# Kernel optimization log

Hardware: AMD Instinct MI355X
Metric: run time of the kernel (lower is better)

The kernel has to match this reference:

```python
import jax, jax.numpy as jnp
import numpy as np

N_SITES, N_BONDS, N_GRAPHS, D = 100000, 800000, 1000, 64
H1, H2 = 64, 32  # megnet_h1, megnet_h2


def _lin(x, w, b):
    return x @ w + b


def _relu_lin(x, w, b):
    return jax.nn.relu(_lin(x, w, b))


def _segment_mean(x, seg, num_segments):
    s = jax.ops.segment_sum(x, seg, num_segments=num_segments)
    cnt = jax.ops.segment_sum(jnp.ones((x.shape[0],), x.dtype), seg, num_segments=num_segments)
    return s / jnp.maximum(cnt, 1.0)[:, None]


def setup_inputs() -> dict:
    key = jax.random.key(0)
    ks = list(jax.random.split(key, 80))
    ki = iter(ks)

    def lp(din, dout):
        w = jax.random.normal(next(ki), (din, dout), jnp.float32) / np.sqrt(din)
        b = jax.random.normal(next(ki), (dout,), jnp.float32) * 0.01
        return w, b

    inp = {}
    inp['sites'] = jax.random.normal(next(ki), (N_SITES, D), jnp.float32)
    inp['bonds'] = jax.random.normal(next(ki), (N_BONDS, D), jnp.float32)
    inp['states'] = jax.random.normal(next(ki), (N_GRAPHS, D), jnp.float32)

    # pre-MEGNet dense layers (D -> H1(=64) -> premegnet_h2(=64))
    for name, din, dout in [('sites_fc1', D, 64), ('sites_fc2', 64, D),
                            ('bonds_fc1', D, 64), ('bonds_fc2', 64, D),
                            ('states_fc1', D, 64), ('states_fc2', 64, D)]:
        w, b = lp(din, dout)
        inp['w_' + name], inp['b_' + name] = w, b
    # bond update MLP: (2D + D + D) -> H1 -> H2 -> D
    for name, din, dout in [('bu_fc1', 4 * D, H1), ('bu_fc2', H1, H2), ('bu_fc3', H2, D)]:
        w, b = lp(din, dout)
        inp['w_' + name], inp['b_' + name] = w, b
    # site update MLP: 3D -> H1 -> H2 -> D
    for name, din, dout in [('su_fc1', 3 * D, H1), ('su_fc2', H1, H2), ('su_fc3', H2, D)]:
        w, b = lp(din, dout)
        inp['w_' + name], inp['b_' + name] = w, b
    # state update MLP: 3D -> H1 -> H2 -> D
    for name, din, dout in [('stu_fc1', 3 * D, H1), ('stu_fc2', H1, H2), ('stu_fc3', H2, D)]:
        w, b = lp(din, dout)
        inp['w_' + name], inp['b_' + name] = w, b

    inp['indices1'] = jax.random.randint(next(ki), (N_BONDS,), 0, N_SITES, jnp.int32)
    inp['indices2'] = jax.random.randint(next(ki), (N_BONDS,), 0, N_SITES, jnp.int32)
    inp['graph_to_sites'] = jnp.sort(jax.random.randint(next(ki), (N_SITES,), 0, N_GRAPHS, jnp.int32))
    inp['graph_to_bonds'] = jnp.sort(jax.random.randint(next(ki), (N_BONDS,), 0, N_GRAPHS, jnp.int32))
    return inp


def _megnet_block(sites, bonds, states,
                  w_sites_fc1, b_sites_fc1, w_sites_fc2, b_sites_fc2,
                  w_bonds_fc1, b_bonds_fc1, w_bonds_fc2, b_bonds_fc2,
                  w_states_fc1, b_states_fc1, w_states_fc2, b_states_fc2,
                  w_bu_fc1, b_bu_fc1, w_bu_fc2, b_bu_fc2, w_bu_fc3, b_bu_fc3,
                  w_su_fc1, b_su_fc1, w_su_fc2, b_su_fc2, w_su_fc3, b_su_fc3,
                  w_stu_fc1, b_stu_fc1, w_stu_fc2, b_stu_fc2, w_stu_fc3, b_stu_fc3,
                  indices1, indices2, graph_to_sites, graph_to_bonds):
    # pre-MEGNet fc layers
    sites = _relu_lin(_relu_lin(sites, w_sites_fc1, b_sites_fc1), w_sites_fc2, b_sites_fc2)
    bonds = _relu_lin(_relu_lin(bonds, w_bonds_fc1, b_bonds_fc1), w_bonds_fc2, b_bonds_fc2)
    states = _relu_lin(_relu_lin(states, w_states_fc1, b_states_fc1), w_states_fc2, b_states_fc2)
    # first_block=True: residual is taken AFTER the fc layers
    init_sites, init_bonds, init_states = sites, bonds, states

    # bond update: gather endpoints + graph state, concat, 3-layer MLP
    v = jnp.concatenate([sites[indices1], sites[indices2], bonds, states[graph_to_bonds]], axis=1)
    v = _relu_lin(v, w_bu_fc1, b_bu_fc1)
    v = _relu_lin(v, w_bu_fc2, b_bu_fc2)
    bonds_new = _relu_lin(v, w_bu_fc3, b_bu_fc3)

    # site update: mean-pool bonds onto their first endpoint
    bonds_pool = _segment_mean(bonds_new, indices1, N_SITES)
    v = jnp.concatenate([bonds_pool, sites, states[graph_to_sites]], axis=1)
    v = _relu_lin(v, w_su_fc1, b_su_fc1)
    v = _relu_lin(v, w_su_fc2, b_su_fc2)
    sites_new = _relu_lin(v, w_su_fc3, b_su_fc3)

    # state update: mean-pool bonds and sites per graph
    bonds_g = _segment_mean(bonds_new, graph_to_bonds, N_GRAPHS)
    sites_g = _segment_mean(sites_new, graph_to_sites, N_GRAPHS)
    v = jnp.concatenate([bonds_g, sites_g, states], axis=1)
    v = _relu_lin(v, w_stu_fc1, b_stu_fc1)
    v = _relu_lin(v, w_stu_fc2, b_stu_fc2)
    states_new = _relu_lin(v, w_stu_fc3, b_stu_fc3)

    return (sites_new + init_sites, bonds_new + init_bonds, states_new + init_states)


def reference(sites, bonds, states,
              w_sites_fc1, b_sites_fc1, w_sites_fc2, b_sites_fc2,
              w_bonds_fc1, b_bonds_fc1, w_bonds_fc2, b_bonds_fc2,
              w_states_fc1, b_states_fc1, w_states_fc2, b_states_fc2,
              w_bu_fc1, b_bu_fc1, w_bu_fc2, b_bu_fc2, w_bu_fc3, b_bu_fc3,
              w_su_fc1, b_su_fc1, w_su_fc2, b_su_fc2, w_su_fc3, b_su_fc3,
              w_stu_fc1, b_stu_fc1, w_stu_fc2, b_stu_fc2, w_stu_fc3, b_stu_fc3,
              indices1, indices2, graph_to_sites, graph_to_bonds):
    return _megnet_block(sites, bonds, states,
                         w_sites_fc1, b_sites_fc1, w_sites_fc2, b_sites_fc2,
                         w_bonds_fc1, b_bonds_fc1, w_bonds_fc2, b_bonds_fc2,
                         w_states_fc1, b_states_fc1, w_states_fc2, b_states_fc2,
                         w_bu_fc1, b_bu_fc1, w_bu_fc2, b_bu_fc2, w_bu_fc3, b_bu_fc3,
                         w_su_fc1, b_su_fc1, w_su_fc2, b_su_fc2, w_su_fc3, b_su_fc3,
                         w_stu_fc1, b_stu_fc1, w_stu_fc2, b_stu_fc2, w_stu_fc3, b_stu_fc3,
                         indices1, indices2, graph_to_sites, graph_to_bonds)
```

## Files before the change

kernel.cpp:

```cpp
#include <hip/hip_runtime.h>

#define N_SITES  100000
#define N_BONDS  800000
#define N_GRAPHS 1000

typedef short bfx8 __attribute__((ext_vector_type(8)));
typedef float fx4  __attribute__((ext_vector_type(4)));

__device__ __forceinline__ bfx8 ldfrag128(const short* buf, int row, int k){
  int off = (row*128 + k*2) ^ ((row&7)<<4);
  return *(const bfx8*)((const char*)buf + off);
}
__device__ __forceinline__ bfx8 ldfrag64(const short* buf, int row, int k){
  int off = (row*64 + k*2) ^ ((row&7)<<4);
  return *(const bfx8*)((const char*)buf + off);
}
__device__ __forceinline__ void stb16_128(short* buf, int row, int col, float v){
  int off = (row*128 + col*2) ^ ((row&7)<<4);
  *(__bf16*)((char*)buf + off) = (__bf16)v;
}
__device__ __forceinline__ float ldb16_128(const short* buf, int row, int col){
  int off = (row*128 + col*2) ^ ((row&7)<<4);
  return (float)*(const __bf16*)((const char*)buf + off);
}
__device__ __forceinline__ void stb16_64(short* buf, int row, int col, float v){
  int off = (row*64 + col*2) ^ ((row&7)<<4);
  *(__bf16*)((char*)buf + off) = (__bf16)v;
}

__device__ __forceinline__ void gemm64(const short* Ab, const short* Bw,
                                       fx4 (&acc)[4][4], int q, int c){
  #pragma unroll
  for (int kt = 0; kt < 2; ++kt){
    int k = kt*32 + q*8;
    bfx8 a0 = ldfrag128(Ab,  0+c, k);
    bfx8 a1 = ldfrag128(Ab, 16+c, k);
    bfx8 a2 = ldfrag128(Ab, 32+c, k);
    bfx8 a3 = ldfrag128(Ab, 48+c, k);
    #pragma unroll
    for (int nt = 0; nt < 4; ++nt){
      bfx8 b = ldfrag128(Bw, nt*16+c, k);
      acc[0][nt] = __builtin_amdgcn_mfma_f32_16x16x32_bf16(a0, b, acc[0][nt], 0,0,0);
      acc[1][nt] = __builtin_amdgcn_mfma_f32_16x16x32_bf16(a1, b, acc[1][nt], 0,0,0);
      acc[2][nt] = __builtin_amdgcn_mfma_f32_16x16x32_bf16(a2, b, acc[2][nt], 0,0,0);
      acc[3][nt] = __builtin_amdgcn_mfma_f32_16x16x32_bf16(a3, b, acc[3][nt], 0,0,0);
    }
  }
}
__device__ __forceinline__ void initbias(fx4 (&acc)[4][4], const float* B, int c){
  #pragma unroll
  for (int nt = 0; nt < 4; ++nt){
    float bv = B[nt*16+c];
    fx4 v = {bv, bv, bv, bv};
    #pragma unroll
    for (int mt = 0; mt < 4; ++mt) acc[mt][nt] = v;
  }
}
__device__ __forceinline__ void wbC128(short* dst, fx4 (&acc)[4][4], int q, int c){
  #pragma unroll
  for (int mt = 0; mt < 4; ++mt)
    #pragma unroll
    for (int nt = 0; nt < 4; ++nt)
      #pragma unroll
      for (int i = 0; i < 4; ++i)
        stb16_128(dst, mt*16+q*4+i, nt*16+c, fmaxf(acc[mt][nt][i], 0.f));
}

template<int CNT>
__device__ __forceinline__ void stage_w(float* dst, const float* __restrict__ src, int tid, int nth){
  for (int i = tid; i < CNT; i += nth) dst[i] = src[i];
}
__device__ __forceinline__ void stage_b(float* dst, const float* __restrict__ src, int n, int tid){
  if (tid < n) dst[tid] = src[tid];
}

template<int K, int N, int R, int XS>
__device__ __forceinline__ void layerR(const float* __restrict__ W,
                                       const float* __restrict__ x,
                                       float* __restrict__ acc, int j)
{
  #pragma unroll
  for (int k = 0; k < K; k += 4){
    float w0 = W[(k+0)*N + j];
    float w1 = W[(k+1)*N + j];
    float w2 = W[(k+2)*N + j];
    float w3 = W[(k+3)*N + j];
    #pragma unroll
    for (int r = 0; r < R; ++r){
      float4 xv = *(const float4*)(x + r*XS + k);
      acc[r] = fmaf(xv.x, w0, acc[r]);
      acc[r] = fmaf(xv.y, w1, acc[r]);
      acc[r] = fmaf(xv.z, w2, acc[r]);
      acc[r] = fmaf(xv.w, w3, acc[r]);
    }
  }
}

__device__ __forceinline__ int lbound(const int* __restrict__ a, int n, int v){
  int lo = 0, hi = n;
  while (lo < hi){ int m = (lo+hi) >> 1; if (a[m] < v) lo = m+1; else hi = m; }
  return lo;
}

__global__ __launch_bounds__(256) void prep_small_kernel(
    const float* __restrict__ states,
    const float* __restrict__ w1, const float* __restrict__ b1,
    const float* __restrict__ w2, const float* __restrict__ b2,
    const float* __restrict__ w_bu1, const float* __restrict__ b_bu1,
    const float* __restrict__ w_su1, const float* __restrict__ b_su1,
    const float* __restrict__ w_stu1, const float* __restrict__ b_stu1,
    float* __restrict__ states2, float* __restrict__ statec_bu,
    float* __restrict__ statec_su, float* __restrict__ statec_stu)
{
  __shared__ float W1[4096], W2[4096], WD[4096], WsuC[4096], WstuC[4096];
  __shared__ float B1[64], B2[64], Bbu[64], Bsu[64], Bstu[64];
  __shared__ alignas(16) float xs[4][64];
  __shared__ alignas(16) float hs[4][64];
  int tid = threadIdx.x;
  stage_w<4096>(W1,    w1,              tid, 256);
  stage_w<4096>(W2,    w2,              tid, 256);
  stage_w<4096>(WD,    w_bu1 + 192*64,  tid, 256);
  stage_w<4096>(WsuC,  w_su1 + 128*64,  tid, 256);
  stage_w<4096>(WstuC, w_stu1 + 128*64, tid, 256);
  stage_b(B1, b1, 64, tid);  stage_b(B2, b2, 64, tid);
  stage_b(Bbu, b_bu1, 64, tid); stage_b(Bsu, b_su1, 64, tid); stage_b(Bstu, b_stu1, 64, tid);
  __syncthreads();
  int w = tid >> 6, lane = tid & 63;
  int g = blockIdx.x*4 + w;
  xs[w][lane] = states[(size_t)g*64 + lane];
  float a = B1[lane];
  layerR<64,64,1,64>(W1, xs[w], &a, lane);
  hs[w][lane] = fmaxf(a, 0.f);
  a = B2[lane];
  layerR<64,64,1,64>(W2, hs[w], &a, lane);
  float s2 = fmaxf(a, 0.f);
  xs[w][lane] = s2;
  size_t o = (size_t)g*64 + lane;
  float abu = Bbu[lane], asu = Bsu[lane], astu = Bstu[lane];
  layerR<64,64,1,64>(WD,    xs[w], &abu,  lane);
  layerR<64,64,1,64>(WsuC,  xs[w], &asu,  lane);
  layerR<64,64,1,64>(WstuC, xs[w], &astu, lane);
  states2[o]    = s2;
  statec_bu[o]  = abu;
  statec_su[o]  = asu;
  statec_stu[o] = astu;
}

__global__ __launch_bounds__(256) void sites_pre_kernel(
    const float* __restrict__ sites,
    const float* __restrict__ w1, const float* __restrict__ b1,
    const float* __restrict__ w2, const float* __restrict__ b2,
    float* __restrict__ sites2)
{
  __shared__ float W1[4096], W2[4096];
  __shared__ float B1[64], B2[64];
  __shared__ alignas(16) float xs[4][4][64];
  __shared__ alignas(16) float hs[4][4][64];
  int tid = threadIdx.x;
  stage_w<4096>(W1, w1, tid, 256);
  stage_w<4096>(W2, w2, tid, 256);
  stage_b(B1, b1, 64, tid); stage_b(B2, b2, 64, tid);
  __syncthreads();
  int w = tid >> 6, lane = tid & 63;
  int wgid = blockIdx.x*4 + w;
  for (int n = 0; n < 7; ++n){
    int G = n*4096 + wgid;
    if (G >= 25000) break;
    #pragma unroll
    for (int r = 0; r < 4; ++r)
      xs[w][r][lane] = sites[((size_t)(4*G + r))*64 + lane];
    {
      float a[4] = {B1[lane], B1[lane], B1[lane], B1[lane]};
      layerR<64,64,4,64>(W1, &xs[w][0][0], a, lane);
      #pragma unroll
      for (int r = 0; r < 4; ++r) hs[w][r][lane] = fmaxf(a[r], 0.f);
    }
    {
      float a[4] = {B2[lane], B2[lane], B2[lane], B2[lane]};
      layerR<64,64,4,64>(W2, &hs[w][0][0], a, lane);
      #pragma unroll
      for (int r = 0; r < 4; ++r)
        sites2[((size_t)(4*G + r))*64 + lane] = fmaxf(a[r], 0.f);
    }
  }
}

__global__ __launch_bounds__(256) void bond_kernel(
    const float* __restrict__ bonds,
    const float* __restrict__ wb1, const float* __restrict__ bb1,
    const float* __restrict__ wb2, const float* __restrict__ bb2,
    const float* __restrict__ w_bu1,
    const float* __restrict__ w_bu2, const float* __restrict__ b_bu2,
    const float* __restrict__ w_bu3, const float* __restrict__ b_bu3,
    const int* __restrict__ idx1, const int* __restrict__ idx2, const int* __restrict__ g2b,
    const float* __restrict__ sites2, const float* __restrict__ statec_bu,
    float* __restrict__ bonds_pool, int* __restrict__ cnt_pool, float* __restrict__ bonds_g,
    float* __restrict__ out_bonds)
{
  __shared__ alignas(16) short WT1[4096], WT2[4096], WTA[4096], WTB[4096], WTC[4096];
  __shared__ alignas(16) short WTU2[2048];
  __shared__ alignas(16) short WTU3[2048];
  __shared__ float BB1[64], BB2[64], BU2[32], BU3[64];
  __shared__ alignas(16) short Xb[4][4096];
  __shared__ alignas(16) short Gb[4][4096];
  __shared__ int I1w[4][64], GGw[4][64];
  int tid = threadIdx.x;
  {
    const float* srcs3[5] = {wb1, wb2, w_bu1, w_bu1 + 64*64, w_bu1 + 128*64};
    short* dsts3[5] = {WT1, WT2, WTA, WTB, WTC};
    #pragma unroll
    for (int m = 0; m < 5; ++m){
      const float* s = srcs3[m]; short* d = dsts3[m];
      for (int i = tid; i < 4096; i += 256){
        int k = i >> 6, n = i & 63;
        int off = (n*128 + k*2) ^ ((n&7)<<4);
        *(__bf16*)((char*)d + off) = (__bf16)s[i];
      }
    }
    for (int i = tid; i < 2048; i += 256){
      int k = i >> 5, n = i & 31;
      int off = (n*128 + k*2) ^ ((n&7)<<4);
      *(__bf16*)((char*)WTU2 + off) = (__bf16)w_bu2[i];
    }
    for (int i = tid; i < 2048; i += 256){
      int k = i >> 6, n = i & 63;
      int off = (n*64 + k*2) ^ ((n&7)<<4);
      *(__bf16*)((char*)WTU3 + off) = (__bf16)w_bu3[i];
    }
    stage_b(BB1, bb1, 64, tid); stage_b(BB2, bb2, 64, tid);
    stage_b(BU2, b_bu2, 32, tid); stage_b(BU3, b_bu3, 64, tid);
  }
  __syncthreads();

  int w = tid >> 6, lane = tid & 63, q = lane >> 4, c = lane & 15;
  int e0 = (blockIdx.x*4 + w) * 64;
  short* X = Xb[w];
  short* G = Gb[w];

  {
    int i1l = idx1[e0 + lane];
    I1w[w][lane] = i1l;
    GGw[w][lane] = g2b[e0 + lane];
    atomicAdd(&cnt_pool[i1l], 1);
  }
  #pragma unroll 8
  for (int r = 0; r < 64; ++r){
    float v = bonds[(size_t)(e0 + r)*64 + lane];
    stb16_128(X, r, lane, v);
  }

  fx4 acc[4][4];
  initbias(acc, BB1, c);
  gemm64(X, WT1, acc, q, c);
  wbC128(G, acc, q, c);
  initbias(acc, BB2, c);
  gemm64(G, WT2, acc, q, c);
  wbC128(X, acc, q, c);

  #pragma unroll 8
  for (int r = 0; r < 64; ++r){
    int i1 = I1w[w][r];
    stb16_128(G, r, lane, sites2[(size_t)i1*64 + lane]);
  }
  #pragma unroll
  for (int mt = 0; mt < 4; ++mt)
    #pragma unroll
    for (int i = 0; i < 4; ++i){
      int g = GGw[w][mt*16 + q*4 + i];
      #pragma unroll
      for (int nt = 0; nt < 4; ++nt)
        acc[mt][nt][i] = statec_bu[(size_t)g*64 + nt*16 + c];
    }
  gemm64(G, WTA, acc, q, c);
  #pragma unroll 8
  for (int r = 0; r < 64; ++r){
    int i2 = idx2[e0 + r];
    stb16_128(G, r, lane, sites2[(size_t)i2*64 + lane]);
  }
  gemm64(G, WTB, acc, q, c);
  gemm64(X, WTC, acc, q, c);
  wbC128(G, acc, q, c);

  {
    fx4 a2[4][2];
    #pragma unroll
    for (int nt = 0; nt < 2; ++nt){
      float bv = BU2[nt*16 + c];
      fx4 v = {bv, bv, bv, bv};
      #pragma unroll
      for (int mt = 0; mt < 4; ++mt) a2[mt][nt] = v;
    }
    #pragma unroll
    for (int kt = 0; kt < 2; ++kt){
      int k = kt*32 + q*8;
      bfx8 f0 = ldfrag128(G,  0+c, k);
      bfx8 f1 = ldfrag128(G, 16+c, k);
      bfx8 f2 = ldfrag128(G, 32+c, k);
      bfx8 f3 = ldfrag128(G, 48+c, k);
      #pragma unroll
      for (int nt = 0; nt < 2; ++nt){
        bfx8 b = ldfrag128(WTU2, nt*16+c, k);
        a2[0][nt] = __builtin_amdgcn_mfma_f32_16x16x32_bf16(f0, b, a2[0][nt], 0,0,0);
        a2[1][nt] = __builtin_amdgcn_mfma_f32_16x16x32_bf16(f1, b, a2[1][nt], 0,0,0);
        a2[2][nt] = __builtin_amdgcn_mfma_f32_16x16x32_bf16(f2, b, a2[2][nt], 0,0,0);
        a2[3][nt] = __builtin_amdgcn_mfma_f32_16x16x32_bf16(f3, b, a2[3][nt], 0,0,0);
      }
    }
    #pragma unroll
    for (int mt = 0; mt < 4; ++mt)
      #pragma unroll
      for (int nt = 0; nt < 2; ++nt)
        #pragma unroll
        for (int i = 0; i < 4; ++i)
          stb16_64(G, mt*16+q*4+i, nt*16+c, fmaxf(a2[mt][nt][i], 0.f));
  }
  {
    initbias(acc, BU3, c);
    int k = q*8;
    bfx8 f0 = ldfrag64(G,  0+c, k);
    bfx8 f1 = ldfrag64(G, 16+c, k);
    bfx8 f2 = ldfrag64(G, 32+c, k);
    bfx8 f3 = ldfrag64(G, 48+c, k);
    #pragma unroll
    for (int nt = 0; nt < 4; ++nt){
      bfx8 b = ldfrag64(WTU3, nt*16+c, k);
      acc[0][nt] = __builtin_amdgcn_mfma_f32_16x16x32_bf16(f0, b, acc[0][nt], 0,0,0);
      acc[1][nt] = __builtin_amdgcn_mfma_f32_16x16x32_bf16(f1, b, acc[1][nt], 0,0,0);
      acc[2][nt] = __builtin_amdgcn_mfma_f32_16x16x32_bf16(f2, b, acc[2][nt], 0,0,0);
      acc[3][nt] = __builtin_amdgcn_mfma_f32_16x16x32_bf16(f3, b, acc[3][nt], 0,0,0);
    }
  }
  #pragma unroll
  for (int nt = 0; nt < 4; ++nt){
    int col = nt*16 + c;
    float ga = 0.f; int cg = -1;
    #pragma unroll
    for (int mt = 0; mt < 4; ++mt){
      #pragma unroll
      for (int i = 0; i < 4; ++i){
        int row = mt*16 + q*4 + i;
        float bn = fmaxf(acc[mt][nt][i], 0.f);
        float b2 = ldb16_128(X, row, col);
        out_bonds[(size_t)(e0 + row)*64 + col] = bn + b2;
        atomicAdd(&bonds_pool[(size_t)I1w[w][row]*64 + col], bn);
        int g = GGw[w][row];
        if (g != cg){
          if (cg >= 0) atomicAdd(&bonds_g[(size_t)cg*64 + col], ga);
          cg = g; ga = 0.f;
        }
        ga += bn;
      }
    }
    if (cg >= 0) atomicAdd(&bonds_g[(size_t)cg*64 + col], ga);
  }
}

__global__ __launch_bounds__(512) void site_kernel(
    const float* __restrict__ sites2, const float* __restrict__ bonds_pool, const int* __restrict__ cnt_pool,
    const int* __restrict__ g2s, const float* __restrict__ statec_su,
    const float* __restrict__ w_su1, const float* __restrict__ w_su2, const float* __restrict__ b_su2,
    const float* __restrict__ w_su3, const float* __restrict__ b_su3,
    float* __restrict__ sites_g, float* __restrict__ out_sites)
{
  __shared__ float W1a[4096], W1b[4096], W2[2048], W3[2048];
  __shared__ float B2s[32], B3s[64];
  __shared__ alignas(16) float P[8][4][64];
  __shared__ alignas(16) float Q[8][4][64];
  __shared__ alignas(16) float H2[8][4][32];
  int tid = threadIdx.x;
  stage_w<4096>(W1a, w_su1,         tid, 512);
  stage_w<4096>(W1b, w_su1 + 64*64, tid, 512);
  stage_w<2048>(W2,  w_su2,         tid, 512);
  stage_w<2048>(W3,  w_su3,         tid, 512);
  stage_b(B2s, b_su2, 32, tid); stage_b(B3s, b_su3, 64, tid);
  __syncthreads();
  int w = tid >> 6, lane = tid & 63;
  int sbase = (blockIdx.x*8 + w)*16;
  if (sbase >= N_SITES) return;
  float gacc = 0.f; int cur_g = -1;
  for (int it = 0; it < 4; ++it){
    int s0 = sbase + it*4;
    int gg[4];
    #pragma unroll
    for (int r = 0; r < 4; ++r){
      int s = s0 + r;
      gg[r] = g2s[s];
      float inv = 1.f / fmaxf((float)cnt_pool[s], 1.f);
      P[w][r][lane] = bonds_pool[(size_t)s*64 + lane] * inv;
      Q[w][r][lane] = sites2[(size_t)s*64 + lane];
    }
    {
      float a[4];
      #pragma unroll
      for (int r = 0; r < 4; ++r) a[r] = statec_su[(size_t)gg[r]*64 + lane];
      layerR<64,64,4,64>(W1a, &P[w][0][0], a, lane);
      layerR<64,64,4,64>(W1b, &Q[w][0][0], a, lane);
      #pragma unroll
      for (int r = 0; r < 4; ++r) P[w][r][lane] = fmaxf(a[r], 0.f);
    }
    {
      int j = lane & 31;
      float a[4] = {B2s[j], B2s[j], B2s[j], B2s[j]};
      layerR<64,32,4,64>(W2, &P[w][0][0], a, j);
      if (lane < 32){
        #pragma unroll
        for (int r = 0; r < 4; ++r) H2[w][r][lane] = fmaxf(a[r], 0.f);
      }
    }
    {
      float a[4] = {B3s[lane], B3s[lane], B3s[lane], B3s[lane]};
      layerR<32,64,4,32>(W3, &H2[w][0][0], a, lane);
      #pragma unroll
      for (int r = 0; r < 4; ++r){
        int s = s0 + r;
        float snew = fmaxf(a[r], 0.f);
        out_sites[(size_t)s*64 + lane] = snew + Q[w][r][lane];
        if (gg[r] != cur_g){
          if (cur_g >= 0) atomicAdd(&sites_g[(size_t)cur_g*64 + lane], gacc);
          cur_g = gg[r]; gacc = 0.f;
        }
        gacc += snew;
      }
    }
  }
  if (cur_g >= 0) atomicAdd(&sites_g[(size_t)cur_g*64 + lane], gacc);
}

__global__ __launch_bounds__(64) void state_kernel(
    const float* __restrict__ states2, const float* __restrict__ bonds_g, const float* __restrict__ sites_g,
    const int* __restrict__ g2b, const int* __restrict__ g2s,
    const float* __restrict__ w_stu1, const float* __restrict__ w_stu2, const float* __restrict__ b_stu2,
    const float* __restrict__ w_stu3, const float* __restrict__ b_stu3,
    const float* __restrict__ statec_stu, float* __restrict__ out_states)
{
  __shared__ float W1a[4096], W1b[4096], W2[2048], W3[2048];
  __shared__ float B2s[32], B3s[64];
  __shared__ alignas(16) float xb[64], xsit[64], hsx[64], h2x[32];
  __shared__ int cnts[2];
  int lane = threadIdx.x; int g = blockIdx.x;
  stage_w<4096>(W1a, w_stu1,         lane, 64);
  stage_w<4096>(W1b, w_stu1 + 64*64, lane, 64);
  stage_w<2048>(W2,  w_stu2,         lane, 64);
  stage_w<2048>(W3,  w_stu3,         lane, 64);
  stage_b(B2s, b_stu2, 32, lane); stage_b(B3s, b_stu3, 64, lane);
  if (lane == 0){
    cnts[0] = lbound(g2b, N_BONDS, g+1) - lbound(g2b, N_BONDS, g);
    cnts[1] = lbound(g2s, N_SITES, g+1) - lbound(g2s, N_SITES, g);
  }
  __syncthreads();
  float invb = 1.f / fmaxf((float)cnts[0], 1.f);
  float invs = 1.f / fmaxf((float)cnts[1], 1.f);
  xb[lane]   = bonds_g[(size_t)g*64 + lane] * invb;
  xsit[lane] = sites_g[(size_t)g*64 + lane] * invs;
  __syncthreads();
  {
    float a = statec_stu[(size_t)g*64 + lane];
    layerR<64,64,1,64>(W1a, xb,   &a, lane);
    layerR<64,64,1,64>(W1b, xsit, &a, lane);
    hsx[lane] = fmaxf(a, 0.f);
  }
  __syncthreads();
  {
    int j = lane & 31;
    float a = B2s[j];
    layerR<64,32,1,64>(W2, hsx, &a, j);
    if (lane < 32) h2x[lane] = fmaxf(a, 0.f);
  }
  __syncthreads();
  {
    float a = B3s[lane];
    layerR<32,64,1,32>(W3, h2x, &a, lane);
    out_states[(size_t)g*64 + lane] = fmaxf(a, 0.f) + states2[(size_t)g*64 + lane];
  }
}

extern "C" void kernel_launch(void* const* d_in, const int* in_sizes, int n_in,
                              void* d_out, int out_size, void* d_ws, size_t ws_size,
                              hipStream_t stream)
{
  const float* sites   = (const float*)d_in[0];
  const float* bonds   = (const float*)d_in[1];
  const float* states  = (const float*)d_in[2];
  const float* w_sites1 = (const float*)d_in[3];  const float* b_sites1 = (const float*)d_in[4];
  const float* w_sites2 = (const float*)d_in[5];  const float* b_sites2 = (const float*)d_in[6];
  const float* w_bonds1 = (const float*)d_in[7];  const float* b_bonds1 = (const float*)d_in[8];
  const float* w_bonds2 = (const float*)d_in[9];  const float* b_bonds2 = (const float*)d_in[10];
  const float* w_states1= (const float*)d_in[11]; const float* b_states1= (const float*)d_in[12];
  const float* w_states2= (const float*)d_in[13]; const float* b_states2= (const float*)d_in[14];
  const float* w_bu1 = (const float*)d_in[15]; const float* b_bu1 = (const float*)d_in[16];
  const float* w_bu2 = (const float*)d_in[17]; const float* b_bu2 = (const float*)d_in[18];
  const float* w_bu3 = (const float*)d_in[19]; const float* b_bu3 = (const float*)d_in[20];
  const float* w_su1 = (const float*)d_in[21]; const float* b_su1 = (const float*)d_in[22];
  const float* w_su2 = (const float*)d_in[23]; const float* b_su2 = (const float*)d_in[24];
  const float* w_su3 = (const float*)d_in[25]; const float* b_su3 = (const float*)d_in[26];
  const float* w_stu1= (const float*)d_in[27]; const float* b_stu1= (const float*)d_in[28];
  const float* w_stu2= (const float*)d_in[29]; const float* b_stu2= (const float*)d_in[30];
  const float* w_stu3= (const float*)d_in[31]; const float* b_stu3= (const float*)d_in[32];
  const int* idx1 = (const int*)d_in[33];
  const int* idx2 = (const int*)d_in[34];
  const int* g2s  = (const int*)d_in[35];
  const int* g2b  = (const int*)d_in[36];

  float* p = (float*)d_ws;
  float* bonds_pool = p;        p += (size_t)N_SITES*64;
  float* bonds_g    = p;        p += (size_t)N_GRAPHS*64;
  float* sites_g    = p;        p += (size_t)N_GRAPHS*64;
  int*   cnt_pool   = (int*)p;  p += N_SITES;
  float* states2    = p;        p += (size_t)N_GRAPHS*64;
  float* statec_bu  = p;        p += (size_t)N_GRAPHS*64;
  float* statec_su  = p;        p += (size_t)N_GRAPHS*64;
  float* statec_stu = p;        p += (size_t)N_GRAPHS*64;

  size_t zero_bytes = ((size_t)N_SITES*64 + 2*(size_t)N_GRAPHS*64 + (size_t)N_SITES) * 4;
  hipMemsetAsync(d_ws, 0, zero_bytes, stream);

  float* out_sites  = (float*)d_out;
  float* out_bonds  = out_sites + (size_t)N_SITES*64;
  float* out_states = out_bonds + (size_t)N_BONDS*64;
  float* sites2     = out_sites;

  hipLaunchKernelGGL(prep_small_kernel, dim3(250), dim3(256), 0, stream,
      states, w_states1, b_states1, w_states2, b_states2,
      w_bu1, b_bu1, w_su1, b_su1, w_stu1, b_stu1,
      states2, statec_bu, statec_su, statec_stu);

  hipLaunchKernelGGL(sites_pre_kernel, dim3(1024), dim3(256), 0, stream,
      sites, w_sites1, b_sites1, w_sites2, b_sites2, sites2);

  hipLaunchKernelGGL(bond_kernel, dim3(3125), dim3(256), 0, stream,
      bonds, w_bonds1, b_bonds1, w_bonds2, b_bonds2,
      w_bu1, w_bu2, b_bu2, w_bu3, b_bu3,
      idx1, idx2, g2b, sites2, statec_bu,
      bonds_pool, cnt_pool, bonds_g, out_bonds);

  hipLaunchKernelGGL(site_kernel, dim3(782), dim3(512), 0, stream,
      sites2, bonds_pool, cnt_pool, g2s, statec_su,
      w_su1, w_su2, b_su2, w_su3, b_su3,
      sites_g, out_sites);

  hipLaunchKernelGGL(state_kernel, dim3(1000), dim3(64), 0, stream,
      states2, bonds_g, sites_g, g2b, g2s,
      w_stu1, w_stu2, b_stu2, w_stu3, b_stu3,
      statec_stu, out_states);
}
```

Measured before the change: 1.085 ms.

## Convert site kernels to MFMA and gather A-fragments directly from global memory

Rewrites sites_pre_kernel and site_kernel to use bf16 MFMA 16x16x32 tiles over 64-row blocks, replacing the scalar FMA layers. The bond kernel now loads A fragments straight from global fp32 rows, including gathered sites2 rows, instead of staging them through LDS. It keeps the small tail weights in registers, drops the second LDS buffer, and re-reads out_bonds for the residual add. The aim is to cut LDS traffic and occupancy pressure and to use the matrix cores throughout. In exchange it adds bf16 rounding in the site path, uncoalesced per-lane row loads, and a global read-back of out_bonds.

```diff
diff --git a/kernel.cpp b/kernel.cpp
--- a/kernel.cpp
+++ b/kernel.cpp
@@ -7,6 +7,8 @@
 typedef short bfx8 __attribute__((ext_vector_type(8)));
 typedef float fx4  __attribute__((ext_vector_type(4)));
 
+__device__ __forceinline__ short b16(float x){ __bf16 h = (__bf16)x; return *(short*)&h; }
+
 __device__ __forceinline__ bfx8 ldfrag128(const short* buf, int row, int k){
   int off = (row*128 + k*2) ^ ((row&7)<<4);
   return *(const bfx8*)((const char*)buf + off);
@@ -19,13 +21,26 @@
   int off = (row*128 + col*2) ^ ((row&7)<<4);
   *(__bf16*)((char*)buf + off) = (__bf16)v;
 }
-__device__ __forceinline__ float ldb16_128(const short* buf, int row, int col){
-  int off = (row*128 + col*2) ^ ((row&7)<<4);
-  return (float)*(const __bf16*)((const char*)buf + off);
-}
 __device__ __forceinline__ void stb16_64(short* buf, int row, int col, float v){
   int off = (row*64 + col*2) ^ ((row&7)<<4);
   *(__bf16*)((char*)buf + off) = (__bf16)v;
+}
+
+__device__ __forceinline__ bfx8 fragG(const float* rp, int k){
+  float4 u = *(const float4*)(rp + k);
+  float4 v = *(const float4*)(rp + k + 4);
+  bfx8 r;
+  r[0]=b16(u.x); r[1]=b16(u.y); r[2]=b16(u.z); r[3]=b16(u.w);
+  r[4]=b16(v.x); r[5]=b16(v.y); r[6]=b16(v.z); r[7]=b16(v.w);
+  return r;
+}
+__device__ __forceinline__ bfx8 fragGs(const float* rp, float s, int k){
+  float4 u = *(const float4*)(rp + k);
+  float4 v = *(const float4*)(rp + k + 4);
+  bfx8 r;
+  r[0]=b16(u.x*s); r[1]=b16(u.y*s); r[2]=b16(u.z*s); r[3]=b16(u.w*s);
+  r[4]=b16(v.x*s); r[5]=b16(v.y*s); r[6]=b16(v.z*s); r[7]=b16(v.w*s);
+  return r;
 }
 
 __device__ __forceinline__ void gemm64(const short* Ab, const short* Bw,
@@ -47,7 +62,45 @@
     }
   }
 }
-__device__ __forceinline__ void initbias(fx4 (&acc)[4][4], const float* B, int c){
+__device__ __forceinline__ void gemmG(const float* const (&rp)[4], const short* Bw,
+                                      fx4 (&acc)[4][4], int q, int c){
+  #pragma unroll
+  for (int kt = 0; kt < 2; ++kt){
+    int k = kt*32 + q*8;
+    bfx8 a0 = fragG(rp[0], k);
+    bfx8 a1 = fragG(rp[1], k);
+    bfx8 a2 = fragG(rp[2], k);
+    bfx8 a3 = fragG(rp[3], k);
+    #pragma unroll
+    for (int nt = 0; nt < 4; ++nt){
+      bfx8 b = ldfrag128(Bw, nt*16+c, k);
+      acc[0][nt] = __builtin_amdgcn_mfma_f32_16x16x32_bf16(a0, b, acc[0][nt], 0,0,0);
+      acc[1][nt] = __builtin_amdgcn_mfma_f32_16x16x32_bf16(a1, b, acc[1][nt], 0,0,0);
+      acc[2][nt] = __builtin_amdgcn_mfma_f32_16x16x32_bf16(a2, b, acc[2][nt], 0,0,0);
+      acc[3][nt] = __builtin_amdgcn_mfma_f32_16x16x32_bf16(a3, b, acc[3][nt], 0,0,0);
+    }
+  }
+}
+__device__ __forceinline__ void gemmGs(const float* const (&rp)[4], const float (&sc)[4],
+                                       const short* Bw, fx4 (&acc)[4][4], int q, int c){
+  #pragma unroll
+  for (int kt = 0; kt < 2; ++kt){
+    int k = kt*32 + q*8;
+    bfx8 a0 = fragGs(rp[0], sc[0], k);
+    bfx8 a1 = fragGs(rp[1], sc[1], k);
+    bfx8 a2 = fragGs(rp[2], sc[2], k);
+    bfx8 a3 = fragGs(rp[3], sc[3], k);
+    #pragma unroll
+    for (int nt = 0; nt < 4; ++nt){
+      bfx8 b = ldfrag128(Bw, nt*16+c, k);
+      acc[0][nt] = __builtin_amdgcn_mfma_f32_16x16x32_bf16(a0, b, acc[0][nt], 0,0,0);
+      acc[1][nt] = __builtin_amdgcn_mfma_f32_16x16x32_bf16(a1, b, acc[1][nt], 0,0,0);
+      acc[2][nt] = __builtin_amdgcn_mfma_f32_16x16x32_bf16(a2, b, acc[2][nt], 0,0,0);
+      acc[3][nt] = __builtin_amdgcn_mfma_f32_16x16x32_bf16(a3, b, acc[3][nt], 0,0,0);
+    }
+  }
+}
+__device__ __forceinline__ void initbiasG(fx4 (&acc)[4][4], const float* B, int c){
   #pragma unroll
   for (int nt = 0; nt < 4; ++nt){
     float bv = B[nt*16+c];
@@ -66,6 +119,87 @@
         stb16_128(dst, mt*16+q*4+i, nt*16+c, fmaxf(acc[mt][nt][i], 0.f));
 }
 
+__device__ __forceinline__ void stage_wt(short* dst, const float* __restrict__ src,
+                                         int tid, int nth){
+  for (int i = tid; i < 4096; i += nth){
+    int k = i >> 6, n = i & 63;
+    int off = (n*128 + k*2) ^ ((n&7)<<4);
+    *(__bf16*)((char*)dst + off) = (__bf16)src[i];
+  }
+}
+
+__device__ __forceinline__ void preload_tail(const float* __restrict__ w2,
+                                             const float* __restrict__ w3,
+                                             bfx8 (&u2)[2][2], bfx8 (&u3)[4],
+                                             int q, int c){
+  #pragma unroll
+  for (int kt = 0; kt < 2; ++kt)
+    #pragma unroll
+    for (int nt = 0; nt < 2; ++nt)
+      #pragma unroll
+      for (int j = 0; j < 8; ++j)
+        u2[kt][nt][j] = b16(w2[(kt*32 + q*8 + j)*32 + nt*16 + c]);
+  #pragma unroll
+  for (int nt = 0; nt < 4; ++nt)
+    #pragma unroll
+    for (int j = 0; j < 8; ++j)
+      u3[nt][j] = b16(w3[(q*8 + j)*64 + nt*16 + c]);
+}
+
+__device__ __forceinline__ void tail3264(short* X, const bfx8 (&u2)[2][2], const bfx8 (&u3)[4],
+                                         const float* __restrict__ b2g,
+                                         const float* __restrict__ b3g,
+                                         fx4 (&acc)[4][4], int q, int c){
+  fx4 a2[4][2];
+  #pragma unroll
+  for (int nt = 0; nt < 2; ++nt){
+    float bv = b2g[nt*16+c];
+    fx4 v = {bv, bv, bv, bv};
+    #pragma unroll
+    for (int mt = 0; mt < 4; ++mt) a2[mt][nt] = v;
+  }
+  #pragma unroll
+  for (int kt = 0; kt < 2; ++kt){
+    int k = kt*32 + q*8;
+    bfx8 f0 = ldfrag128(X,  0+c, k);
+    bfx8 f1 = ldfrag128(X, 16+c, k);
+    bfx8 f2 = ldfrag128(X, 32+c, k);
+    bfx8 f3 = ldfrag128(X, 48+c, k);
+    #pragma unroll
+    for (int nt = 0; nt < 2; ++nt){
+      a2[0][nt] = __builtin_amdgcn_mfma_f32_16x16x32_bf16(f0, u2[kt][nt], a2[0][nt], 0,0,0);
+      a2[1][nt] = __builtin_amdgcn_mfma_f32_16x16x32_bf16(f1, u2[kt][nt], a2[1][nt], 0,0,0);
+      a2[2][nt] = __builtin_amdgcn_mfma_f32_16x16x32_bf16(f2, u2[kt][nt], a2[2][nt], 0,0,0);
+      a2[3][nt] = __builtin_amdgcn_mfma_f32_16x16x32_bf16(f3, u2[kt][nt], a2[3][nt], 0,0,0);
+    }
+  }
+  #pragma unroll
+  for (int mt = 0; mt < 4; ++mt)
+    #pragma unroll
+    for (int nt = 0; nt < 2; ++nt)
+      #pragma unroll
+      for (int i = 0; i < 4; ++i)
+        stb16_64(X, mt*16+q*4+i, nt*16+c, fmaxf(a2[mt][nt][i], 0.f));
+  #pragma unroll
+  for (int nt = 0; nt < 4; ++nt){
+    float bv = b3g[nt*16+c];
+    fx4 v = {bv, bv, bv, bv};
+    #pragma unroll
+    for (int mt = 0; mt < 4; ++mt) acc[mt][nt] = v;
+  }
+  bfx8 g0 = ldfrag64(X,  0+c, q*8);
+  bfx8 g1 = ldfrag64(X, 16+c, q*8);
+  bfx8 g2 = ldfrag64(X, 32+c, q*8);
+  bfx8 g3 = ldfrag64(X, 48+c, q*8);
+  #pragma unroll
+  for (int nt = 0; nt < 4; ++nt){
+    acc[0][nt] = __builtin_amdgcn_mfma_f32_16x16x32_bf16(g0, u3[nt], acc[0][nt], 0,0,0);
+    acc[1][nt] = __builtin_amdgcn_mfma_f32_16x16x32_bf16(g1, u3[nt], acc[1][nt], 0,0,0);
+    acc[2][nt] = __builtin_amdgcn_mfma_f32_16x16x32_bf16(g2, u3[nt], acc[2][nt], 0,0,0);
+    acc[3][nt] = __builtin_amdgcn_mfma_f32_16x16x32_bf16(g3, u3[nt], acc[3][nt], 0,0,0);
+  }
+}
+
 template<int CNT>
 __device__ __forceinline__ void stage_w(float* dst, const float* __restrict__ src, int tid, int nth){
   for (int i = tid; i < CNT; i += nth) dst[i] = src[i];
@@ -73,7 +207,6 @@
 __device__ __forceinline__ void stage_b(float* dst, const float* __restrict__ src, int n, int tid){
   if (tid < n) dst[tid] = src[tid];
 }
-
 template<int K, int N, int R, int XS>
 __device__ __forceinline__ void layerR(const float* __restrict__ W,
                                        const float* __restrict__ x,
@@ -95,7 +228,6 @@
     }
   }
 }
-
 __device__ __forceinline__ int lbound(const int* __restrict__ a, int n, int v){
   int lo = 0, hi = n;
   while (lo < hi){ int m = (lo+hi) >> 1; if (a[m] < v) lo = m+1; else hi = m; }
@@ -152,37 +284,40 @@
     const float* __restrict__ w2, const float* __restrict__ b2,
     float* __restrict__ sites2)
 {
-  __shared__ float W1[4096], W2[4096];
-  __shared__ float B1[64], B2[64];
-  __shared__ alignas(16) float xs[4][4][64];
-  __shared__ alignas(16) float hs[4][4][64];
+  __shared__ alignas(16) short WT1[4096], WT2[4096];
+  __shared__ alignas(16) short Xb[4][4096];
   int tid = threadIdx.x;
-  stage_w<4096>(W1, w1, tid, 256);
-  stage_w<4096>(W2, w2, tid, 256);
-  stage_b(B1, b1, 64, tid); stage_b(B2, b2, 64, tid);
-  __syncthreads();
-  int w = tid >> 6, lane = tid & 63;
-  int wgid = blockIdx.x*4 + w;
-  for (int n = 0; n < 7; ++n){
-    int G = n*4096 + wgid;
-    if (G >= 25000) break;
-    #pragma unroll
-    for (int r = 0; r < 4; ++r)
-      xs[w][r][lane] = sites[((size_t)(4*G + r))*64 + lane];
-    {
-      float a[4] = {B1[lane], B1[lane], B1[lane], B1[lane]};
-      layerR<64,64,4,64>(W1, &xs[w][0][0], a, lane);
-      #pragma unroll
-      for (int r = 0; r < 4; ++r) hs[w][r][lane] = fmaxf(a[r], 0.f);
-    }
-    {
-      float a[4] = {B2[lane], B2[lane], B2[lane], B2[lane]};
-      layerR<64,64,4,64>(W2, &hs[w][0][0], a, lane);
-      #pragma unroll
-      for (int r = 0; r < 4; ++r)
-        sites2[((size_t)(4*G + r))*64 + lane] = fmaxf(a[r], 0.f);
-    }
-  }
+  stage_wt(WT1, w1, tid, 256);
+  stage_wt(WT2, w2, tid, 256);
+  __syncthreads();
+  int w = tid >> 6, lane = tid & 63, q = lane >> 4, c = lane & 15;
+  int c0 = (blockIdx.x*4 + w) * 64;
+  if (c0 >= N_SITES) return;
+  short* X = Xb[w];
+  fx4 acc[4][4];
+  initbiasG(acc, b1, c);
+  {
+    const float* rp[4];
+    #pragma unroll
+    for (int mt = 0; mt < 4; ++mt){
+      int r = c0 + mt*16 + c; if (r > N_SITES-1) r = N_SITES-1;
+      rp[mt] = sites + (size_t)r*64;
+    }
+    gemmG(rp, WT1, acc, q, c);
+  }
+  wbC128(X, acc, q, c);
+  initbiasG(acc, b2, c);
+  gemm64(X, WT2, acc, q, c);
+  #pragma unroll
+  for (int mt = 0; mt < 4; ++mt)
+    #pragma unroll
+    for (int nt = 0; nt < 4; ++nt)
+      #pragma unroll
+      for (int i = 0; i < 4; ++i){
+        int row = c0 + mt*16 + q*4 + i;
+        if (row < N_SITES)
+          sites2[(size_t)row*64 + nt*16 + c] = fmaxf(acc[mt][nt][i], 0.f);
+      }
 }
 
 __global__ __launch_bounds__(256) void bond_kernel(
@@ -198,232 +333,186 @@
     float* __restrict__ out_bonds)
 {
   __shared__ alignas(16) short WT1[4096], WT2[4096], WTA[4096], WTB[4096], WTC[4096];
-  __shared__ alignas(16) short WTU2[2048];
-  __shared__ alignas(16) short WTU3[2048];
-  __shared__ float BB1[64], BB2[64], BU2[32], BU3[64];
   __shared__ alignas(16) short Xb[4][4096];
-  __shared__ alignas(16) short Gb[4][4096];
-  __shared__ int I1w[4][64], GGw[4][64];
   int tid = threadIdx.x;
-  {
-    const float* srcs3[5] = {wb1, wb2, w_bu1, w_bu1 + 64*64, w_bu1 + 128*64};
-    short* dsts3[5] = {WT1, WT2, WTA, WTB, WTC};
-    #pragma unroll
-    for (int m = 0; m < 5; ++m){
-      const float* s = srcs3[m]; short* d = dsts3[m];
-      for (int i = tid; i < 4096; i += 256){
-        int k = i >> 6, n = i & 63;
-        int off = (n*128 + k*2) ^ ((n&7)<<4);
-        *(__bf16*)((char*)d + off) = (__bf16)s[i];
-      }
-    }
-    for (int i = tid; i < 2048; i += 256){
-      int k = i >> 5, n = i & 31;
-      int off = (n*128 + k*2) ^ ((n&7)<<4);
-      *(__bf16*)((char*)WTU2 + off) = (__bf16)w_bu2[i];
-    }
-    for (int i = tid; i < 2048; i += 256){
-      int k = i >> 6, n = i & 63;
-      int off = (n*64 + k*2) ^ ((n&7)<<4);
-      *(__bf16*)((char*)WTU3 + off) = (__bf16)w_bu3[i];
-    }
-    stage_b(BB1, bb1, 64, tid); stage_b(BB2, bb2, 64, tid);
-    stage_b(BU2, b_bu2, 32, tid); stage_b(BU3, b_bu3, 64, tid);
-  }
-  __syncthreads();
-
+  stage_wt(WT1, wb1,            tid, 256);
+  stage_wt(WT2, wb2,            tid, 256);
+  stage_wt(WTA, w_bu1,          tid, 256);
+  stage_wt(WTB, w_bu1 + 64*64,  tid, 256);
+  stage_wt(WTC, w_bu1 + 128*64, tid, 256);
+  __syncthreads();
   int w = tid >> 6, lane = tid & 63, q = lane >> 4, c = lane & 15;
   int e0 = (blockIdx.x*4 + w) * 64;
   short* X = Xb[w];
-  short* G = Gb[w];
-
-  {
-    int i1l = idx1[e0 + lane];
-    I1w[w][lane] = i1l;
-    GGw[w][lane] = g2b[e0 + lane];
-    atomicAdd(&cnt_pool[i1l], 1);
-  }
-  #pragma unroll 8
-  for (int r = 0; r < 64; ++r){
-    float v = bonds[(size_t)(e0 + r)*64 + lane];
-    stb16_128(X, r, lane, v);
-  }
+
+  bfx8 u2[2][2], u3[4];
+  preload_tail(w_bu2, w_bu3, u2, u3, q, c);
+
+  atomicAdd(&cnt_pool[idx1[e0 + lane]], 1);
+
+  int gr[4][4];
+  #pragma unroll
+  for (int mt = 0; mt < 4; ++mt)
+    #pragma unroll
+    for (int i = 0; i < 4; ++i)
+      gr[mt][i] = g2b[e0 + mt*16 + q*4 + i];
 
   fx4 acc[4][4];
-  initbias(acc, BB1, c);
-  gemm64(X, WT1, acc, q, c);
-  wbC128(G, acc, q, c);
-  initbias(acc, BB2, c);
-  gemm64(G, WT2, acc, q, c);
+  initbiasG(acc, bb1, c);
+  {
+    const float* rp[4];
+    #pragma unroll
+    for (int mt = 0; mt < 4; ++mt) rp[mt] = bonds + (size_t)(e0 + mt*16 + c)*64;
+    gemmG(rp, WT1, acc, q, c);
+  }
   wbC128(X, acc, q, c);
-
-  #pragma unroll 8
-  for (int r = 0; r < 64; ++r){
-    int i1 = I1w[w][r];
-    stb16_128(G, r, lane, sites2[(size_t)i1*64 + lane]);
-  }
-  #pragma unroll
-  for (int mt = 0; mt < 4; ++mt)
-    #pragma unroll
-    for (int i = 0; i < 4; ++i){
-      int g = GGw[w][mt*16 + q*4 + i];
+  initbiasG(acc, bb2, c);
+  gemm64(X, WT2, acc, q, c);
+  #pragma unroll
+  for (int mt = 0; mt < 4; ++mt)
+    #pragma unroll
+    for (int nt = 0; nt < 4; ++nt)
+      #pragma unroll
+      for (int i = 0; i < 4; ++i){
+        float b2v = fmaxf(acc[mt][nt][i], 0.f);
+        int row = mt*16 + q*4 + i, col = nt*16 + c;
+        out_bonds[(size_t)(e0 + row)*64 + col] = b2v;
+        stb16_128(X, row, col, b2v);
+      }
+  #pragma unroll
+  for (int mt = 0; mt < 4; ++mt)
+    #pragma unroll
+    for (int i = 0; i < 4; ++i)
       #pragma unroll
       for (int nt = 0; nt < 4; ++nt)
-        acc[mt][nt][i] = statec_bu[(size_t)g*64 + nt*16 + c];
-    }
-  gemm64(G, WTA, acc, q, c);
-  #pragma unroll 8
-  for (int r = 0; r < 64; ++r){
-    int i2 = idx2[e0 + r];
-    stb16_128(G, r, lane, sites2[(size_t)i2*64 + lane]);
-  }
-  gemm64(G, WTB, acc, q, c);
+        acc[mt][nt][i] = statec_bu[(size_t)gr[mt][i]*64 + nt*16 + c];
+  {
+    const float* rp[4];
+    #pragma unroll
+    for (int mt = 0; mt < 4; ++mt) rp[mt] = sites2 + (size_t)idx1[e0 + mt*16 + c]*64;
+    gemmG(rp, WTA, acc, q, c);
+  }
+  {
+    const float* rp[4];
+    #pragma unroll
+    for (int mt = 0; mt < 4; ++mt) rp[mt] = sites2 + (size_t)idx2[e0 + mt*16 + c]*64;
+    gemmG(rp, WTB, acc, q, c);
+  }
   gemm64(X, WTC, acc, q, c);
-  wbC128(G, acc, q, c);
-
-  {
-    fx4 a2[4][2];
-    #pragma unroll
-    for (int nt = 0; nt < 2; ++nt){
-      float bv = BU2[nt*16 + c];
-      fx4 v = {bv, bv, bv, bv};
-      #pragma unroll
-      for (int mt = 0; mt < 4; ++mt) a2[mt][nt] = v;
-    }
-    #pragma unroll
-    for (int kt = 0; kt < 2; ++kt){
-      int k = kt*32 + q*8;
-      bfx8 f0 = ldfrag128(G,  0+c, k);
-      bfx8 f1 = ldfrag128(G, 16+c, k);
-      bfx8 f2 = ldfrag128(G, 32+c, k);
-      bfx8 f3 = ldfrag128(G, 48+c, k);
-      #pragma unroll
-      for (int nt = 0; nt < 2; ++nt){
-        bfx8 b = ldfrag128(WTU2, nt*16+c, k);
-        a2[0][nt] = __builtin_amdgcn_mfma_f32_16x16x32_bf16(f0, b, a2[0][nt], 0,0,0);
-        a2[1][nt] = __builtin_amdgcn_mfma_f32_16x16x32_bf16(f1, b, a2[1][nt], 0,0,0);
-        a2[2][nt] = __builtin_amdgcn_mfma_f32_16x16x32_bf16(f2, b, a2[2][nt], 0,0,0);
-        a2[3][nt] = __builtin_amdgcn_mfma_f32_16x16x32_bf16(f3, b, a2[3][nt], 0,0,0);
-      }
-    }
-    #pragma unroll
-    for (int mt = 0; mt < 4; ++mt)
-      #pragma unroll
-      for (int nt = 0; nt < 2; ++nt)
-        #pragma unroll
-        for (int i = 0; i < 4; ++i)
-          stb16_64(G, mt*16+q*4+i, nt*16+c, fmaxf(a2[mt][nt][i], 0.f));
-  }
-  {
-    initbias(acc, BU3, c);
-    int k = q*8;
-    bfx8 f0 = ldfrag64(G,  0+c, k);
-    bfx8 f1 = ldfrag64(G, 16+c, k);
-    bfx8 f2 = ldfrag64(G, 32+c, k);
-    bfx8 f3 = ldfrag64(G, 48+c, k);
-    #pragma unroll
-    for (int nt = 0; nt < 4; ++nt){
-      bfx8 b = ldfrag64(WTU3, nt*16+c, k);
-      acc[0][nt] = __builtin_amdgcn_mfma_f32_16x16x32_bf16(f0, b, acc[0][nt], 0,0,0);
-      acc[1][nt] = __builtin_amdgcn_mfma_f32_16x16x32_bf16(f1, b, acc[1][nt], 0,0,0);
-      acc[2][nt] = __builtin_amdgcn_mfma_f32_16x16x32_bf16(f2, b, acc[2][nt], 0,0,0);
-      acc[3][nt] = __builtin_amdgcn_mfma_f32_16x16x32_bf16(f3, b, acc[3][nt], 0,0,0);
-    }
-  }
+  wbC128(X, acc, q, c);
+  tail3264(X, u2, u3, b_bu2, b_bu3, acc, q, c);
+  int i1r[4][4];
+  #pragma unroll
+  for (int mt = 0; mt < 4; ++mt)
+    #pragma unroll
+    for (int i = 0; i < 4; ++i)
+      i1r[mt][i] = idx1[e0 + mt*16 + q*4 + i];
   #pragma unroll
   for (int nt = 0; nt < 4; ++nt){
     int col = nt*16 + c;
     float ga = 0.f; int cg = -1;
     #pragma unroll
-    for (int mt = 0; mt < 4; ++mt){
+    for (int mt = 0; mt < 4; ++mt)
       #pragma unroll
       for (int i = 0; i < 4; ++i){
         int row = mt*16 + q*4 + i;
         float bn = fmaxf(acc[mt][nt][i], 0.f);
-        float b2 = ldb16_128(X, row, col);
-        out_bonds[(size_t)(e0 + row)*64 + col] = bn + b2;
-        atomicAdd(&bonds_pool[(size_t)I1w[w][row]*64 + col], bn);
-        int g = GGw[w][row];
+        size_t o = (size_t)(e0 + row)*64 + col;
+        out_bonds[o] = bn + out_bonds[o];
+        atomicAdd(&bonds_pool[(size_t)i1r[mt][i]*64 + col], bn);
+        int g = gr[mt][i];
         if (g != cg){
           if (cg >= 0) atomicAdd(&bonds_g[(size_t)cg*64 + col], ga);
           cg = g; ga = 0.f;
         }
         ga += bn;
       }
-    }
     if (cg >= 0) atomicAdd(&bonds_g[(size_t)cg*64 + col], ga);
   }
 }
 
-__global__ __launch_bounds__(512) void site_kernel(
+__global__ __launch_bounds__(256) void site_kernel(
     const float* __restrict__ sites2, const float* __restrict__ bonds_pool, const int* __restrict__ cnt_pool,
     const int* __restrict__ g2s, const float* __restrict__ statec_su,
     const float* __restrict__ w_su1, const float* __restrict__ w_su2, const float* __restrict__ b_su2,
     const float* __restrict__ w_su3, const float* __restrict__ b_su3,
     float* __restrict__ sites_g, float* __restrict__ out_sites)
 {
-  __shared__ float W1a[4096], W1b[4096], W2[2048], W3[2048];
-  __shared__ float B2s[32], B3s[64];
-  __shared__ alignas(16) float P[8][4][64];
-  __shared__ alignas(16) float Q[8][4][64];
-  __shared__ alignas(16) float H2[8][4][32];
+  __shared__ alignas(16) short WTa[4096], WTb[4096];
+  __shared__ alignas(16) short Xb[4][4096];
   int tid = threadIdx.x;
-  stage_w<4096>(W1a, w_su1,         tid, 512);
-  stage_w<4096>(W1b, w_su1 + 64*64, tid, 512);
-  stage_w<2048>(W2,  w_su2,         tid, 512);
-  stage_w<2048>(W3,  w_su3,         tid, 512);
-  stage_b(B2s, b_su2, 32, tid); stage_b(B3s, b_su3, 64, tid);
-  __syncthreads();
-  int w = tid >> 6, lane = tid & 63;
-  int sbase = (blockIdx.x*8 + w)*16;
-  if (sbase >= N_SITES) return;
-  float gacc = 0.f; int cur_g = -1;
-  for (int it = 0; it < 4; ++it){
-    int s0 = sbase + it*4;
-    int gg[4];
-    #pragma unroll
-    for (int r = 0; r < 4; ++r){
-      int s = s0 + r;
-      gg[r] = g2s[s];
-      float inv = 1.f / fmaxf((float)cnt_pool[s], 1.f);
-      P[w][r][lane] = bonds_pool[(size_t)s*64 + lane] * inv;
-      Q[w][r][lane] = sites2[(size_t)s*64 + lane];
-    }
-    {
-      float a[4];
-      #pragma unroll
-      for (int r = 0; r < 4; ++r) a[r] = statec_su[(size_t)gg[r]*64 + lane];
-      layerR<64,64,4,64>(W1a, &P[w][0][0], a, lane);
-      layerR<64,64,4,64>(W1b, &Q[w][0][0], a, lane);
-      #pragma unroll
-      for (int r = 0; r < 4; ++r) P[w][r][lane] = fmaxf(a[r], 0.f);
-    }
-    {
-      int j = lane & 31;
-      float a[4] = {B2s[j], B2s[j], B2s[j], B2s[j]};
-      layerR<64,32,4,64>(W2, &P[w][0][0], a, j);
-      if (lane < 32){
-        #pragma unroll
-        for (int r = 0; r < 4; ++r) H2[w][r][lane] = fmaxf(a[r], 0.f);
+  stage_wt(WTa, w_su1,         tid, 256);
+  stage_wt(WTb, w_su1 + 64*64, tid, 256);
+  __syncthreads();
+  int w = tid >> 6, lane = tid & 63, q = lane >> 4, c = lane & 15;
+  int s0 = (blockIdx.x*4 + w) * 64;
+  if (s0 >= N_SITES) return;
+  short* X = Xb[w];
+
+  bfx8 u2[2][2], u3[4];
+  preload_tail(w_su2, w_su3, u2, u3, q, c);
+
+  int gr[4][4];
+  #pragma unroll
+  for (int mt = 0; mt < 4; ++mt)
+    #pragma unroll
+    for (int i = 0; i < 4; ++i){
+      int r = s0 + mt*16 + q*4 + i; if (r > N_SITES-1) r = N_SITES-1;
+      gr[mt][i] = g2s[r];
+    }
+  fx4 acc[4][4];
+  #pragma unroll
+  for (int mt = 0; mt < 4; ++mt)
+    #pragma unroll
+    for (int i = 0; i < 4; ++i)
+      #pragma unroll
+      for (int nt = 0; nt < 4; ++nt)
+        acc[mt][nt][i] = statec_su[(size_t)gr[mt][i]*64 + nt*16 + c];
+  {
+    const float* rp[4]; float sc[4];
+    #pragma unroll
+    for (int mt = 0; mt < 4; ++mt){
+      int r = s0 + mt*16 + c; if (r > N_SITES-1) r = N_SITES-1;
+      rp[mt] = bonds_pool + (size_t)r*64;
+      sc[mt] = 1.f / fmaxf((float)cnt_pool[r], 1.f);
+    }
+    gemmGs(rp, sc, WTa, acc, q, c);
+  }
+  {
+    const float* rp[4];
+    #pragma unroll
+    for (int mt = 0; mt < 4; ++mt){
+      int r = s0 + mt*16 + c; if (r > N_SITES-1) r = N_SITES-1;
+      rp[mt] = sites2 + (size_t)r*64;
+    }
+    gemmG(rp, WTb, acc, q, c);
+  }
+  wbC128(X, acc, q, c);
+  tail3264(X, u2, u3, b_su2, b_su3, acc, q, c);
+  #pragma unroll
+  for (int nt = 0; nt < 4; ++nt){
+    int col = nt*16 + c;
+    float ga = 0.f; int cg = -1;
+    #pragma unroll
+    for (int mt = 0; mt < 4; ++mt)
+      #pragma unroll
+      for (int i = 0; i < 4; ++i){
+        int s = s0 + mt*16 + q*4 + i;
+        if (s < N_SITES){
+          float sn = fmaxf(acc[mt][nt][i], 0.f);
+          size_t o = (size_t)s*64 + col;
+          float s2 = sites2[o];
+          out_sites[o] = sn + s2;
+          int g = gr[mt][i];
+          if (g != cg){
+            if (cg >= 0) atomicAdd(&sites_g[(size_t)cg*64 + col], ga);
+            cg = g; ga = 0.f;
+          }
+          ga += sn;
+        }
       }
-    }
-    {
-      float a[4] = {B3s[lane], B3s[lane], B3s[lane], B3s[lane]};
-      layerR<32,64,4,32>(W3, &H2[w][0][0], a, lane);
-      #pragma unroll
-      for (int r = 0; r < 4; ++r){
-        int s = s0 + r;
-        float snew = fmaxf(a[r], 0.f);
-        out_sites[(size_t)s*64 + lane] = snew + Q[w][r][lane];
-        if (gg[r] != cur_g){
-          if (cur_g >= 0) atomicAdd(&sites_g[(size_t)cur_g*64 + lane], gacc);
-          cur_g = gg[r]; gacc = 0.f;
-        }
-        gacc += snew;
-      }
-    }
-  }
-  if (cur_g >= 0) atomicAdd(&sites_g[(size_t)cur_g*64 + lane], gacc);
+    if (cg >= 0) atomicAdd(&sites_g[(size_t)cg*64 + col], ga);
+  }
 }
 
 __global__ __launch_bounds__(64) void state_kernel(
@@ -524,7 +613,7 @@
       w_bu1, b_bu1, w_su1, b_su1, w_stu1, b_stu1,
       states2, statec_bu, statec_su, statec_stu);
 
-  hipLaunchKernelGGL(sites_pre_kernel, dim3(1024), dim3(256), 0, stream,
+  hipLaunchKernelGGL(sites_pre_kernel, dim3(391), dim3(256), 0, stream,
       sites, w_sites1, b_sites1, w_sites2, b_sites2, sites2);
 
   hipLaunchKernelGGL(bond_kernel, dim3(3125), dim3(256), 0, stream,
@@ -533,7 +622,7 @@
       idx1, idx2, g2b, sites2, statec_bu,
       bonds_pool, cnt_pool, bonds_g, out_bonds);
 
-  hipLaunchKernelGGL(site_kernel, dim3(782), dim3(512), 0, stream,
+  hipLaunchKernelGGL(site_kernel, dim3(391), dim3(256), 0, stream,
       sites2, bonds_pool, cnt_pool, g2s, statec_su,
       w_su1, w_su2, b_su2, w_su3, b_su3,
       sites_g, out_sites);
```

Result: slower. 1.223 ms (+12.7%).
